# Kernel tuning notes

Hardware: AMD Instinct MI355X
Metric: run time of the kernel (lower is better)

## Reference

```python
import jax, jax.numpy as jnp
import numpy as np


def setup_inputs() -> dict:
    key0 = jax.random.key(0)
    kq, kk, kv = jax.random.split(key0, 3)
    B, S, H, KVH, D = 1, 4096, 8, 2, 64
    return {
        "query": jax.random.normal(kq, (B, S, H, D), dtype=jnp.float32),
        "key": jax.random.normal(kk, (B, S, KVH, D), dtype=jnp.float32),
        "value": jax.random.normal(kv, (B, S, KVH, D), dtype=jnp.float32),
    }


def _ring_attn_single(query, key, value):
    # world_size == 1 (dist uninitialized): ring loop is a single local step
    # with query_offset == key_offset == 0.
    B, S, H, D = query.shape
    KVH = key.shape[2]
    scale = D ** -0.5
    # [B, H, S, D]
    q = query.transpose(0, 2, 1, 3)
    k = key.transpose(0, 2, 1, 3)
    v = value.transpose(0, 2, 1, 3)
    if KVH != H:
        rep = H // KVH
        k = jnp.repeat(k, rep, axis=1)  # repeat_interleave on head dim
        v = jnp.repeat(v, rep, axis=1)
    logits = jnp.einsum("bhqd,bhkd->bhqk", q, k) * scale
    pos = jnp.arange(S)
    causal = pos[:, None] < pos[None, :]  # mask future keys
    logits = jnp.where(causal[None, None], -jnp.inf, logits)
    w = jax.nn.softmax(logits, axis=-1)  # [B, H, S, S]
    attn_out = jnp.einsum("bhqk,bhkd->bhqd", w, v)
    cw = jnp.sum(w, axis=-1, keepdims=True)  # chunk softmax mass (== 1)
    out = attn_out * cw / (cw + 1e-8)  # weight-accumulation renorm
    return out.transpose(0, 2, 1, 3)  # [B, S, H, D]


def reference(query, key, value):
    return _ring_attn_single(query, key, value)
```

## Files before the change

### kernel.cpp

```cpp
#include <hip/hip_runtime.h>
#include <hip/hip_bf16.h>


#define S_LEN 4096
#define H_Q   8
#define H_KV  2
#define DH    64
#define BM    64
#define BN    64
#define PITCH 72
#define NEG_BIG (-1e30f)
#define CS (0.125f * 1.44269504088896340736f)

#define CHUNK 12
#define NTR   204
#define KB_SH (S_LEN * H_KV * DH)
#define OB_FLOATS ((size_t)NTR * H_Q * BM * DH)
#define L_FLOATS  ((size_t)NTR * H_Q * BM)
#define WS_NEED ((size_t)(2 * KB_SH) * 2 + (OB_FLOATS + L_FLOATS) * 4)

typedef __attribute__((ext_vector_type(8))) short bf16x8;
typedef __attribute__((ext_vector_type(4))) short s16x4;
typedef __attribute__((ext_vector_type(4))) float f32x4;
typedef __attribute__((ext_vector_type(4))) unsigned int u32x4;

__device__ __forceinline__ short bf(float x) {
    return __builtin_bit_cast(short, __float2bfloat16(x));
}
__device__ __forceinline__ unsigned int pk2(float lo, float hi) {
    return (unsigned int)(unsigned short)bf(lo)
         | ((unsigned int)(unsigned short)bf(hi) << 16);
}

__global__ __launch_bounds__(256)
void ring_attn_prepass(const float* __restrict__ K, const float* __restrict__ V,
                       short* __restrict__ Kb, short* __restrict__ Vt) {
    const int b = blockIdx.x;
    const int t = threadIdx.x;
    if (b < 512) {
        const int i = (b * 256 + t) * 4;
        float4 kv = *(const float4*)(K + i);
        *(unsigned int*)(Kb + i)     = pk2(kv.x, kv.y);
        *(unsigned int*)(Kb + i + 2) = pk2(kv.z, kv.w);
    } else {
        __shared__ short T[DH * PITCH];
        const int bb  = b - 512;
        const int kvh = bb >> 6;
        const int s0  = (bb & 63) * 64;
        {
            const int r  = t >> 2;
            const int dq = (t & 3) * 16;
            const float* vp = V + ((s0 + r) * H_KV + kvh) * DH + dq;
            float4 a0 = *(const float4*)(vp);
            float4 a1 = *(const float4*)(vp + 4);
            float4 a2 = *(const float4*)(vp + 8);
            float4 a3 = *(const float4*)(vp + 12);
            float e[16] = {a0.x,a0.y,a0.z,a0.w, a1.x,a1.y,a1.z,a1.w,
                           a2.x,a2.y,a2.z,a2.w, a3.x,a3.y,a3.z,a3.w};
#pragma unroll
            for (int i = 0; i < 16; ++i)
                T[(dq + i) * PITCH + r] = bf(e[i]);
        }
        __syncthreads();
        {
            const int d  = t >> 2;
            const int sq = (t & 3) * 16;
            bf16x8 x0 = *(const bf16x8*)(&T[d * PITCH + sq]);
            bf16x8 x1 = *(const bf16x8*)(&T[d * PITCH + sq + 8]);
            short* op = Vt + (kvh * DH + d) * S_LEN + s0 + sq;
            *(bf16x8*)(op)     = x0;
            *(bf16x8*)(op + 8) = x1;
        }
    }
}

template <bool SPLIT>
__global__ __launch_bounds__(256)
void ring_attn_fwd(const float* __restrict__ Q, const short* __restrict__ Kb,
                   const short* __restrict__ Vt, float* __restrict__ O,
                   float* __restrict__ Obuf, float* __restrict__ Lbuf) {
    const int bid = blockIdx.x;
    const int h   = bid & 7;
    int qt, nch, jbeg, jend, tr0;
    if (SPLIT) {
        const int tr = (NTR - 1) - (bid >> 3);
        int b, base;
        if (tr < 12)       { b = 0; base = 0; }
        else if (tr < 36)  { b = 1; base = 12; }
        else if (tr < 72)  { b = 2; base = 36; }
        else if (tr < 120) { b = 3; base = 72; }
        else if (tr < 180) { b = 4; base = 120; }
        else               { b = 5; base = 180; }
        const int u  = tr - base;
        const int qq = u / (b + 1);
        const int ch = u - qq * (b + 1);
        qt   = 12 * b + qq;
        nch  = b + 1;
        tr0  = base + qq * (b + 1);
        jbeg = ch * CHUNK;
        jend = min(qt + 1, jbeg + CHUNK);
    } else {
        qt = (S_LEN / BM - 1) - (bid >> 3);
        nch = 1; jbeg = 0; jend = qt + 1; tr0 = 0;
    }
    const int kvh = h >> 2;

    __shared__ short Ks[BN * PITCH];
    __shared__ short Vs[DH * PITCH];

    const int tid  = threadIdx.x;
    const int w    = tid >> 6;
    const int lane = tid & 63;
    const int c    = lane & 15;
    const int q    = lane >> 4;

    bf16x8 qf0, qf1;
    {
        const int qg = qt * BM + w * 16 + c;
        const float* qp = Q + (qg * H_Q + h) * DH + q * 8;
        float4 a0 = *(const float4*)(qp);
        float4 a1 = *(const float4*)(qp + 4);
        float4 b0 = *(const float4*)(qp + 32);
        float4 b1 = *(const float4*)(qp + 36);
        qf0 = bf16x8{bf(a0.x*CS), bf(a0.y*CS), bf(a0.z*CS), bf(a0.w*CS),
                     bf(a1.x*CS), bf(a1.y*CS), bf(a1.z*CS), bf(a1.w*CS)};
        qf1 = bf16x8{bf(b0.x*CS), bf(b0.y*CS), bf(b0.z*CS), bf(b0.w*CS),
                     bf(b1.x*CS), bf(b1.y*CS), bf(b1.z*CS), bf(b1.w*CS)};
    }

    f32x4 acc[4] = {f32x4{0,0,0,0}, f32x4{0,0,0,0}, f32x4{0,0,0,0}, f32x4{0,0,0,0}};
    float l_lane = 0.0f;

    const int rr = tid >> 3;
    const int cc = (tid & 7) * 8;

    for (int j = jbeg; j < jend; ++j) {
        __syncthreads();
#pragma unroll
        for (int p = 0; p < 2; ++p) {
            const int n = p * 32 + rr;
            bf16x8 x = *(const bf16x8*)(Kb + ((j * BN + n) * H_KV + kvh) * DH + cc);
            *(bf16x8*)(&Ks[n * PITCH + cc]) = x;
        }
#pragma unroll
        for (int p = 0; p < 2; ++p) {
            const int d = p * 32 + rr;
            bf16x8 x = *(const bf16x8*)(Vt + (kvh * DH + d) * S_LEN + j * BN + cc);
            *(bf16x8*)(&Vs[d * PITCH + cc]) = x;
        }
        __syncthreads();

        f32x4 s[4] = {f32x4{0,0,0,0}, f32x4{0,0,0,0}, f32x4{0,0,0,0}, f32x4{0,0,0,0}};
#pragma unroll
        for (int nt = 0; nt < 4; ++nt) {
            bf16x8 kf0 = *(const bf16x8*)(&Ks[(nt * 16 + c) * PITCH + q * 8]);
            bf16x8 kf1 = *(const bf16x8*)(&Ks[(nt * 16 + c) * PITCH + q * 8 + 32]);
            s[nt] = __builtin_amdgcn_mfma_f32_16x16x32_bf16(kf0, qf0, s[nt], 0, 0, 0);
            s[nt] = __builtin_amdgcn_mfma_f32_16x16x32_bf16(kf1, qf1, s[nt], 0, 0, 0);
        }

        if (j == qt) {
            const int qrl = w * 16 + c;
#pragma unroll
            for (int nt = 0; nt < 4; ++nt) {
                const int kl = nt * 16 + q * 4;
#pragma unroll
                for (int r = 0; r < 4; ++r)
                    if (kl + r > qrl) s[nt][r] = NEG_BIG;
            }
        }

#pragma unroll
        for (int nt = 0; nt < 4; ++nt)
#pragma unroll
            for (int r = 0; r < 4; ++r) {
                const float p = exp2f(s[nt][r]);
                s[nt][r] = p;
                l_lane += p;
            }

        u32x4 w0 = {pk2(s[0][0], s[0][1]), pk2(s[0][2], s[0][3]),
                    pk2(s[1][0], s[1][1]), pk2(s[1][2], s[1][3])};
        u32x4 w1 = {pk2(s[2][0], s[2][1]), pk2(s[2][2], s[2][3]),
                    pk2(s[3][0], s[3][1]), pk2(s[3][2], s[3][3])};
        bf16x8 pf0 = __builtin_bit_cast(bf16x8, w0);
        bf16x8 pf1 = __builtin_bit_cast(bf16x8, w1);

#pragma unroll
        for (int dt = 0; dt < 4; ++dt) {
            const int base = (dt * 16 + c) * PITCH;
            s16x4 v0 = *(const s16x4*)(&Vs[base + 4 * q]);
            s16x4 v1 = *(const s16x4*)(&Vs[base + 16 + 4 * q]);
            s16x4 v2 = *(const s16x4*)(&Vs[base + 32 + 4 * q]);
            s16x4 v3 = *(const s16x4*)(&Vs[base + 48 + 4 * q]);
            bf16x8 vf0 = bf16x8{v0[0],v0[1],v0[2],v0[3], v1[0],v1[1],v1[2],v1[3]};
            bf16x8 vf1 = bf16x8{v2[0],v2[1],v2[2],v2[3], v3[0],v3[1],v3[2],v3[3]};
            acc[dt] = __builtin_amdgcn_mfma_f32_16x16x32_bf16(pf0, vf0, acc[dt], 0, 0, 0);
            acc[dt] = __builtin_amdgcn_mfma_f32_16x16x32_bf16(pf1, vf1, acc[dt], 0, 0, 0);
        }
    }

    float t2 = l_lane;
    t2 += __shfl_xor(t2, 16);
    t2 += __shfl_xor(t2, 32);
    float lr[4];
#pragma unroll
    for (int r = 0; r < 4; ++r)
        lr[r] = __shfl(t2, q * 4 + r);

    if (!SPLIT || nch == 1) {
        const int qg = qt * BM + w * 16;
#pragma unroll
        for (int r = 0; r < 4; ++r) {
            const float inv = 1.0f / lr[r];
            float* op = O + ((qg + q * 4 + r) * H_Q + h) * DH + c;
#pragma unroll
            for (int dt = 0; dt < 4; ++dt)
                op[dt * 16] = acc[dt][r] * inv;
        }
    } else {
        const int slot = (tr0 + jbeg / CHUNK) * 8 + h;
        float* ob = Obuf + (size_t)slot * (BM * DH);
#pragma unroll
        for (int r = 0; r < 4; ++r) {
            const int rin = w * 16 + q * 4 + r;
#pragma unroll
            for (int dt = 0; dt < 4; ++dt)
                ob[rin * DH + dt * 16 + c] = acc[dt][r];
        }
        if (lane < 16)
            Lbuf[slot * BM + w * 16 + lane] = t2;
    }
}

__global__ __launch_bounds__(256)
void ring_attn_combine(const float* __restrict__ Obuf, const float* __restrict__ Lbuf,
                       float* __restrict__ O) {
    const int gid  = blockIdx.x * 256 + threadIdx.x;
    const int d    = gid & 63;
    const int h    = (gid >> 6) & 7;
    const int srow = 768 + (gid >> 9);
    const int qt   = srow >> 6;
    const int rin  = srow & 63;
    const int b    = qt / 12;
    static const int bases[6] = {0, 12, 36, 72, 120, 180};
    const int nch  = b + 1;
    const int tr0  = bases[b] + (qt - 12 * b) * nch;

    float num = 0.0f, den = 0.0f;
    for (int ch = 0; ch < nch; ++ch) {
        const int slot = (tr0 + ch) * 8 + h;
        den += Lbuf[slot * BM + rin];
        num += Obuf[(size_t)slot * (BM * DH) + rin * DH + d];
    }
    O[(srow * H_Q + h) * DH + d] = num / den;
}

extern "C" void kernel_launch(void* const* d_in, const int* in_sizes, int n_in,
                              void* d_out, int out_size, void* d_ws, size_t ws_size,
                              hipStream_t stream) {
    const float* Q = (const float*)d_in[0];
    const float* K = (const float*)d_in[1];
    const float* V = (const float*)d_in[2];
    float* O  = (float*)d_out;
    short* Kb = (short*)d_ws;
    short* Vt = Kb + KB_SH;
    float* Obuf = (float*)(Vt + KB_SH);
    float* Lbuf = Obuf + OB_FLOATS;

    ring_attn_prepass<<<640, 256, 0, stream>>>(K, V, Kb, Vt);
    if (ws_size >= WS_NEED) {
        ring_attn_fwd<true><<<NTR * H_Q, 256, 0, stream>>>(Q, Kb, Vt, O, Obuf, Lbuf);
        ring_attn_combine<<<(S_LEN - 768) * H_Q * DH / 256, 256, 0, stream>>>(Obuf, Lbuf, O);
    } else {
        ring_attn_fwd<false><<<(S_LEN / BM) * H_Q, 256, 0, stream>>>(Q, Kb, Vt, O, Obuf, Lbuf);
    }
}
```

Measured before the change: 119.2 us.

## Process two 64-row query subtiles per block to reuse K/V tiles

```diff
diff --git a/kernel.cpp b/kernel.cpp
--- a/kernel.cpp
+++ b/kernel.cpp
@@ -6,17 +6,16 @@
 #define H_Q   8
 #define H_KV  2
 #define DH    64
-#define BM    64
 #define BN    64
 #define PITCH 72
 #define NEG_BIG (-1e30f)
 #define CS (0.125f * 1.44269504088896340736f)
 
 #define CHUNK 12
-#define NTR   204
+#define NTR   102
 #define KB_SH (S_LEN * H_KV * DH)
-#define OB_FLOATS ((size_t)NTR * H_Q * BM * DH)
-#define L_FLOATS  ((size_t)NTR * H_Q * BM)
+#define OB_FLOATS ((size_t)NTR * H_Q * 128 * DH)
+#define L_FLOATS  ((size_t)NTR * H_Q * 128)
 #define WS_NEED ((size_t)(2 * KB_SH) * 2 + (OB_FLOATS + L_FLOATS) * 4)
 
 typedef __attribute__((ext_vector_type(8))) short bf16x8;
@@ -63,11 +62,15 @@
         }
         __syncthreads();
         {
-            const int d  = t >> 2;
-            const int sq = (t & 3) * 16;
-            bf16x8 x0 = *(const bf16x8*)(&T[d * PITCH + sq]);
-            bf16x8 x1 = *(const bf16x8*)(&T[d * PITCH + sq + 8]);
-            short* op = Vt + (kvh * DH + d) * S_LEN + s0 + sq;
+            const int d = t >> 2;
+            const int q = t & 3;
+            s16x4 g0 = *(const s16x4*)(&T[d * PITCH + 4 * q]);
+            s16x4 g1 = *(const s16x4*)(&T[d * PITCH + 16 + 4 * q]);
+            s16x4 g2 = *(const s16x4*)(&T[d * PITCH + 32 + 4 * q]);
+            s16x4 g3 = *(const s16x4*)(&T[d * PITCH + 48 + 4 * q]);
+            bf16x8 x0 = bf16x8{g0[0],g0[1],g0[2],g0[3], g1[0],g1[1],g1[2],g1[3]};
+            bf16x8 x1 = bf16x8{g2[0],g2[1],g2[2],g2[3], g3[0],g3[1],g3[2],g3[3]};
+            short* op = Vt + (kvh * DH + d) * S_LEN + s0 + 16 * q;
             *(bf16x8*)(op)     = x0;
             *(bf16x8*)(op + 8) = x1;
         }
@@ -75,7 +78,7 @@
 }
 
 template <bool SPLIT>
-__global__ __launch_bounds__(256)
+__global__ __launch_bounds__(256, 4)
 void ring_attn_fwd(const float* __restrict__ Q, const short* __restrict__ Kb,
                    const short* __restrict__ Vt, float* __restrict__ O,
                    float* __restrict__ Obuf, float* __restrict__ Lbuf) {
@@ -85,23 +88,23 @@
     if (SPLIT) {
         const int tr = (NTR - 1) - (bid >> 3);
         int b, base;
-        if (tr < 12)       { b = 0; base = 0; }
-        else if (tr < 36)  { b = 1; base = 12; }
-        else if (tr < 72)  { b = 2; base = 36; }
-        else if (tr < 120) { b = 3; base = 72; }
-        else if (tr < 180) { b = 4; base = 120; }
-        else               { b = 5; base = 180; }
+        if (tr < 6)       { b = 0; base = 0; }
+        else if (tr < 18) { b = 1; base = 6; }
+        else if (tr < 36) { b = 2; base = 18; }
+        else if (tr < 60) { b = 3; base = 36; }
+        else if (tr < 90) { b = 4; base = 60; }
+        else              { b = 5; base = 90; }
         const int u  = tr - base;
         const int qq = u / (b + 1);
         const int ch = u - qq * (b + 1);
-        qt   = 12 * b + qq;
+        qt   = 6 * b + qq;
         nch  = b + 1;
         tr0  = base + qq * (b + 1);
         jbeg = ch * CHUNK;
-        jend = min(qt + 1, jbeg + CHUNK);
-    } else {
-        qt = (S_LEN / BM - 1) - (bid >> 3);
-        nch = 1; jbeg = 0; jend = qt + 1; tr0 = 0;
+        jend = min(2 * qt + 2, jbeg + CHUNK);
+    } else {
+        qt = 31 - (bid >> 3);
+        nch = 1; jbeg = 0; jend = 2 * qt + 2; tr0 = 0;
     }
     const int kvh = h >> 2;
 
@@ -114,22 +117,23 @@
     const int c    = lane & 15;
     const int q    = lane >> 4;
 
-    bf16x8 qf0, qf1;
-    {
-        const int qg = qt * BM + w * 16 + c;
+    bf16x8 qf[2][2];
+#pragma unroll
+    for (int st = 0; st < 2; ++st) {
+        const int qg = qt * 128 + st * 64 + w * 16 + c;
         const float* qp = Q + (qg * H_Q + h) * DH + q * 8;
         float4 a0 = *(const float4*)(qp);
         float4 a1 = *(const float4*)(qp + 4);
         float4 b0 = *(const float4*)(qp + 32);
         float4 b1 = *(const float4*)(qp + 36);
-        qf0 = bf16x8{bf(a0.x*CS), bf(a0.y*CS), bf(a0.z*CS), bf(a0.w*CS),
-                     bf(a1.x*CS), bf(a1.y*CS), bf(a1.z*CS), bf(a1.w*CS)};
-        qf1 = bf16x8{bf(b0.x*CS), bf(b0.y*CS), bf(b0.z*CS), bf(b0.w*CS),
-                     bf(b1.x*CS), bf(b1.y*CS), bf(b1.z*CS), bf(b1.w*CS)};
-    }
-
-    f32x4 acc[4] = {f32x4{0,0,0,0}, f32x4{0,0,0,0}, f32x4{0,0,0,0}, f32x4{0,0,0,0}};
-    float l_lane = 0.0f;
+        qf[st][0] = bf16x8{bf(a0.x*CS), bf(a0.y*CS), bf(a0.z*CS), bf(a0.w*CS),
+                           bf(a1.x*CS), bf(a1.y*CS), bf(a1.z*CS), bf(a1.w*CS)};
+        qf[st][1] = bf16x8{bf(b0.x*CS), bf(b0.y*CS), bf(b0.z*CS), bf(b0.w*CS),
+                           bf(b1.x*CS), bf(b1.y*CS), bf(b1.z*CS), bf(b1.w*CS)};
+    }
+
+    f32x4 acc[2][4] = {};
+    float l_lane[2] = {0.f, 0.f};
 
     const int rr = tid >> 3;
     const int cc = (tid & 7) * 8;
@@ -150,86 +154,95 @@
         }
         __syncthreads();
 
-        f32x4 s[4] = {f32x4{0,0,0,0}, f32x4{0,0,0,0}, f32x4{0,0,0,0}, f32x4{0,0,0,0}};
-#pragma unroll
-        for (int nt = 0; nt < 4; ++nt) {
-            bf16x8 kf0 = *(const bf16x8*)(&Ks[(nt * 16 + c) * PITCH + q * 8]);
-            bf16x8 kf1 = *(const bf16x8*)(&Ks[(nt * 16 + c) * PITCH + q * 8 + 32]);
-            s[nt] = __builtin_amdgcn_mfma_f32_16x16x32_bf16(kf0, qf0, s[nt], 0, 0, 0);
-            s[nt] = __builtin_amdgcn_mfma_f32_16x16x32_bf16(kf1, qf1, s[nt], 0, 0, 0);
-        }
-
-        if (j == qt) {
-            const int qrl = w * 16 + c;
+        bf16x8 pf[2][2];
+#pragma unroll
+        for (int st = 0; st < 2; ++st) {
+            f32x4 s[4] = {};
 #pragma unroll
             for (int nt = 0; nt < 4; ++nt) {
-                const int kl = nt * 16 + q * 4;
-#pragma unroll
-                for (int r = 0; r < 4; ++r)
-                    if (kl + r > qrl) s[nt][r] = NEG_BIG;
-            }
-        }
-
-#pragma unroll
-        for (int nt = 0; nt < 4; ++nt)
+                bf16x8 kf0 = *(const bf16x8*)(&Ks[(nt * 16 + c) * PITCH + q * 8]);
+                bf16x8 kf1 = *(const bf16x8*)(&Ks[(nt * 16 + c) * PITCH + q * 8 + 32]);
+                s[nt] = __builtin_amdgcn_mfma_f32_16x16x32_bf16(kf0, qf[st][0], s[nt], 0, 0, 0);
+                s[nt] = __builtin_amdgcn_mfma_f32_16x16x32_bf16(kf1, qf[st][1], s[nt], 0, 0, 0);
+            }
+            if (j >= 2 * qt + st) {
+                const int koff = (j - 2 * qt - st) * 64;
+                const int qrl  = w * 16 + c;
+#pragma unroll
+                for (int nt = 0; nt < 4; ++nt) {
+                    const int kl = koff + nt * 16 + q * 4;
+#pragma unroll
+                    for (int r = 0; r < 4; ++r)
+                        if (kl + r > qrl) s[nt][r] = NEG_BIG;
+                }
+            }
+#pragma unroll
+            for (int nt = 0; nt < 4; ++nt)
+#pragma unroll
+                for (int r = 0; r < 4; ++r) {
+                    const float p = exp2f(s[nt][r]);
+                    s[nt][r] = p;
+                    l_lane[st] += p;
+                }
+            u32x4 w0 = {pk2(s[0][0], s[0][1]), pk2(s[0][2], s[0][3]),
+                        pk2(s[1][0], s[1][1]), pk2(s[1][2], s[1][3])};
+            u32x4 w1 = {pk2(s[2][0], s[2][1]), pk2(s[2][2], s[2][3]),
+                        pk2(s[3][0], s[3][1]), pk2(s[3][2], s[3][3])};
+            pf[st][0] = __builtin_bit_cast(bf16x8, w0);
+            pf[st][1] = __builtin_bit_cast(bf16x8, w1);
+        }
+
+#pragma unroll
+        for (int dt = 0; dt < 4; ++dt) {
+            const int base = (dt * 16 + c) * PITCH + 16 * q;
+            bf16x8 vf0 = *(const bf16x8*)(&Vs[base]);
+            bf16x8 vf1 = *(const bf16x8*)(&Vs[base + 8]);
+            acc[0][dt] = __builtin_amdgcn_mfma_f32_16x16x32_bf16(pf[0][0], vf0, acc[0][dt], 0, 0, 0);
+            acc[0][dt] = __builtin_amdgcn_mfma_f32_16x16x32_bf16(pf[0][1], vf1, acc[0][dt], 0, 0, 0);
+            acc[1][dt] = __builtin_amdgcn_mfma_f32_16x16x32_bf16(pf[1][0], vf0, acc[1][dt], 0, 0, 0);
+            acc[1][dt] = __builtin_amdgcn_mfma_f32_16x16x32_bf16(pf[1][1], vf1, acc[1][dt], 0, 0, 0);
+        }
+    }
+
+    float lr[2][4];
+#pragma unroll
+    for (int st = 0; st < 2; ++st) {
+        float t2 = l_lane[st];
+        t2 += __shfl_xor(t2, 16);
+        t2 += __shfl_xor(t2, 32);
+        l_lane[st] = t2;
+#pragma unroll
+        for (int r = 0; r < 4; ++r)
+            lr[st][r] = __shfl(t2, q * 4 + r);
+    }
+
+    if (!SPLIT || nch == 1) {
+#pragma unroll
+        for (int st = 0; st < 2; ++st)
 #pragma unroll
             for (int r = 0; r < 4; ++r) {
-                const float p = exp2f(s[nt][r]);
-                s[nt][r] = p;
-                l_lane += p;
-            }
-
-        u32x4 w0 = {pk2(s[0][0], s[0][1]), pk2(s[0][2], s[0][3]),
-                    pk2(s[1][0], s[1][1]), pk2(s[1][2], s[1][3])};
-        u32x4 w1 = {pk2(s[2][0], s[2][1]), pk2(s[2][2], s[2][3]),
-                    pk2(s[3][0], s[3][1]), pk2(s[3][2], s[3][3])};
-        bf16x8 pf0 = __builtin_bit_cast(bf16x8, w0);
-        bf16x8 pf1 = __builtin_bit_cast(bf16x8, w1);
-
-#pragma unroll
-        for (int dt = 0; dt < 4; ++dt) {
-            const int base = (dt * 16 + c) * PITCH;
-            s16x4 v0 = *(const s16x4*)(&Vs[base + 4 * q]);
-            s16x4 v1 = *(const s16x4*)(&Vs[base + 16 + 4 * q]);
-            s16x4 v2 = *(const s16x4*)(&Vs[base + 32 + 4 * q]);
-            s16x4 v3 = *(const s16x4*)(&Vs[base + 48 + 4 * q]);
-            bf16x8 vf0 = bf16x8{v0[0],v0[1],v0[2],v0[3], v1[0],v1[1],v1[2],v1[3]};
-            bf16x8 vf1 = bf16x8{v2[0],v2[1],v2[2],v2[3], v3[0],v3[1],v3[2],v3[3]};
-            acc[dt] = __builtin_amdgcn_mfma_f32_16x16x32_bf16(pf0, vf0, acc[dt], 0, 0, 0);
-            acc[dt] = __builtin_amdgcn_mfma_f32_16x16x32_bf16(pf1, vf1, acc[dt], 0, 0, 0);
-        }
-    }
-
-    float t2 = l_lane;
-    t2 += __shfl_xor(t2, 16);
-    t2 += __shfl_xor(t2, 32);
-    float lr[4];
-#pragma unroll
-    for (int r = 0; r < 4; ++r)
-        lr[r] = __shfl(t2, q * 4 + r);
-
-    if (!SPLIT || nch == 1) {
-        const int qg = qt * BM + w * 16;
-#pragma unroll
-        for (int r = 0; r < 4; ++r) {
-            const float inv = 1.0f / lr[r];
-            float* op = O + ((qg + q * 4 + r) * H_Q + h) * DH + c;
-#pragma unroll
-            for (int dt = 0; dt < 4; ++dt)
-                op[dt * 16] = acc[dt][r] * inv;
-        }
+                const float inv = 1.0f / lr[st][r];
+                const int row = qt * 128 + st * 64 + w * 16 + q * 4 + r;
+                float* op = O + (row * H_Q + h) * DH + c;
+#pragma unroll
+                for (int dt = 0; dt < 4; ++dt)
+                    op[dt * 16] = acc[st][dt][r] * inv;
+            }
     } else {
         const int slot = (tr0 + jbeg / CHUNK) * 8 + h;
-        float* ob = Obuf + (size_t)slot * (BM * DH);
-#pragma unroll
-        for (int r = 0; r < 4; ++r) {
-            const int rin = w * 16 + q * 4 + r;
-#pragma unroll
-            for (int dt = 0; dt < 4; ++dt)
-                ob[rin * DH + dt * 16 + c] = acc[dt][r];
-        }
-        if (lane < 16)
-            Lbuf[slot * BM + w * 16 + lane] = t2;
+        float* ob = Obuf + (size_t)slot * (128 * DH);
+#pragma unroll
+        for (int st = 0; st < 2; ++st) {
+#pragma unroll
+            for (int r = 0; r < 4; ++r) {
+                const int rin = st * 64 + w * 16 + q * 4 + r;
+#pragma unroll
+                for (int dt = 0; dt < 4; ++dt)
+                    ob[rin * DH + dt * 16 + c] = acc[st][dt][r];
+            }
+            if (lane < 16)
+                Lbuf[slot * 128 + st * 64 + w * 16 + lane] = l_lane[st];
+        }
     }
 }
 
@@ -240,18 +253,22 @@
     const int d    = gid & 63;
     const int h    = (gid >> 6) & 7;
     const int srow = 768 + (gid >> 9);
-    const int qt   = srow >> 6;
-    const int rin  = srow & 63;
-    const int b    = qt / 12;
-    static const int bases[6] = {0, 12, 36, 72, 120, 180};
-    const int nch  = b + 1;
-    const int tr0  = bases[b] + (qt - 12 * b) * nch;
+    const int qt   = srow >> 7;
+    const int rin  = srow & 127;
+    int b, base;
+    if (qt < 12)      { b = 1; base = 6; }
+    else if (qt < 18) { b = 2; base = 18; }
+    else if (qt < 24) { b = 3; base = 36; }
+    else if (qt < 30) { b = 4; base = 60; }
+    else              { b = 5; base = 90; }
+    const int nch = b + 1;
+    const int tr0 = base + (qt - 6 * b) * nch;
 
     float num = 0.0f, den = 0.0f;
     for (int ch = 0; ch < nch; ++ch) {
         const int slot = (tr0 + ch) * 8 + h;
-        den += Lbuf[slot * BM + rin];
-        num += Obuf[(size_t)slot * (BM * DH) + rin * DH + d];
+        den += Lbuf[slot * 128 + rin];
+        num += Obuf[(size_t)slot * (128 * DH) + rin * DH + d];
     }
     O[(srow * H_Q + h) * DH + d] = num / den;
 }
@@ -273,6 +290,6 @@
         ring_attn_fwd<true><<<NTR * H_Q, 256, 0, stream>>>(Q, Kb, Vt, O, Obuf, Lbuf);
         ring_attn_combine<<<(S_LEN - 768) * H_Q * DH / 256, 256, 0, stream>>>(Obuf, Lbuf, O);
     } else {
-        ring_attn_fwd<false><<<(S_LEN / BM) * H_Q, 256, 0, stream>>>(Q, Kb, Vt, O, Obuf, Lbuf);
-    }
-}
+        ring_attn_fwd<false><<<32 * H_Q, 256, 0, stream>>>(Q, Kb, Vt, O, Obuf, Lbuf);
+    }
+}
```

Result: faster. 116.5 us (-2.2%).
